# Performance work log

Measured on AMD Instinct MI355X. Metric: run time of the kernel, lower is better.

Reference implementation:

```python
import jax, jax.numpy as jnp
import numpy as np

H = 256          # h_dim
SEQ_LEN = 10     # max history length
B = 2048         # number of queries with non-empty history
N = 327680       # total flattened neighbors across all (query, timestep) segments
NUM_SEG = B * SEQ_LEN
NUM_ENT = 20000
NUM_REL = 200


def setup_inputs() -> dict:
    key = jax.random.key(0)
    ks = jax.random.split(key, 9)
    s = jax.random.randint(ks[0], (B,), 0, NUM_ENT)
    r = jax.random.randint(ks[1], (B,), 0, NUM_REL)
    nbr_ids = jax.random.randint(ks[2], (N,), 0, NUM_ENT)
    seg_ids = jnp.sort(jax.random.randint(ks[3], (N,), 0, NUM_SEG))
    ent_embeds = jax.random.normal(ks[4], (NUM_ENT, H), dtype=jnp.float32)
    rel_embeds = jax.random.normal(ks[5], (NUM_REL, H), dtype=jnp.float32)
    W_attn = jax.random.normal(ks[6], (3 * H, H), dtype=jnp.float32) * 0.05
    b_attn = jax.random.normal(ks[7], (H,), dtype=jnp.float32) * 0.05
    v_s = jax.random.normal(ks[8], (H, 1), dtype=jnp.float32) * 0.05
    return {"s": s, "r": r, "nbr_ids": nbr_ids, "seg_ids": seg_ids,
            "ent_embeds": ent_embeds, "rel_embeds": rel_embeds,
            "W_attn": W_attn, "b_attn": b_attn, "v_s": v_s}


def reference(s, r, nbr_ids, seg_ids, ent_embeds, rel_embeds, W_attn, b_attn, v_s):
    # Per-neighbor gathers. Each neighbor belongs to segment seg = q*SEQ_LEN + t.
    q = seg_ids // SEQ_LEN                              # query index per neighbor [N]
    em = ent_embeds[nbr_ids]                            # [N, H] neighbor embeddings
    s_emb = ent_embeds[s]                               # [B, H]
    r_emb = rel_embeds[r]                               # [B, H]
    ss = s_emb[q]                                       # [N, H]
    rr = r_emb[q]                                       # [N, H]
    # Score: tanh(Linear(3H -> H)) @ v_s  -> scalar per neighbor
    x = jnp.concatenate([em, ss, rr], axis=1)           # [N, 3H]
    scores = (jnp.tanh(x @ W_attn + b_attn) @ v_s)[:, 0]  # [N]
    # Segment softmax over neighbors within each (query, timestep) segment.
    m = jax.ops.segment_max(scores, seg_ids, num_segments=NUM_SEG)  # [S]
    e = jnp.exp(scores - m[seg_ids])                    # [N]
    denom = jax.ops.segment_sum(e, seg_ids, num_segments=NUM_SEG)   # [S]
    w = e / denom[seg_ids]                              # [N]
    # Weighted sum of neighbor embeddings per segment (scatter-reduce).
    agg = jax.ops.segment_sum(w[:, None] * em, seg_ids, num_segments=NUM_SEG)  # [S, H]
    counts = jax.ops.segment_sum(jnp.ones_like(scores), seg_ids, num_segments=NUM_SEG)
    mask = (counts > 0).astype(em.dtype).reshape(B, SEQ_LEN, 1)     # present timesteps
    agg = agg.reshape(B, SEQ_LEN, H)
    ss_t = jnp.broadcast_to(s_emb[:, None, :], (B, SEQ_LEN, H))
    rr_t = jnp.broadcast_to(r_emb[:, None, :], (B, SEQ_LEN, H))
    # Padded [B, SEQ_LEN, 3H] sequence tensor (rows for empty segments are zero,
    # matching the torch code's zero-initialized padded tensor). Dropout p=0.0.
    out = jnp.concatenate([agg, ss_t, rr_t], axis=2) * mask
    return out
```

## Files before the change

### kernel.cpp

```cpp
#include <hip/hip_runtime.h>
#include <hip/hip_bf16.h>

#define H 256
#define SEQ 10
#define C2LOG2E 2.8853900817779268f
#define LOG2E 1.4426950408889634f

typedef __attribute__((ext_vector_type(8))) short bf16x8;
typedef __attribute__((ext_vector_type(4))) float f32x4;

__device__ __forceinline__ unsigned short f2bf(float x) {
    union { float f; unsigned u; } v; v.f = x;
    unsigned r = v.u + 0x7fff + ((v.u >> 16) & 1);
    return (unsigned short)(r >> 16);
}
__device__ __forceinline__ float bf2f(unsigned short b) {
    union { unsigned u; float f; } v; v.u = ((unsigned)b) << 16;
    return v.f;
}
__device__ __forceinline__ float fexp2(float x) {
    return __builtin_amdgcn_exp2f(x);
}

__global__ void prep_kernel(const float* __restrict__ W,
                            unsigned short* __restrict__ Wt,
                            const int* __restrict__ seg_ids,
                            int* __restrict__ seg_start,
                            int nWt, int n, int num_seg) {
    if ((int)blockIdx.x < nWt) {
        int idx = blockIdx.x * 256 + threadIdx.x;
        if (idx >= H * 3 * H) return;
        int nn = idx / (3 * H), k = idx % (3 * H);
        Wt[idx] = f2bf(C2LOG2E * W[k * H + nn]);
    } else {
        int j = (blockIdx.x - nWt) * 256 + threadIdx.x;
        if (j >= n) return;
        int cur = seg_ids[j];
        int prev = (j == 0) ? -1 : seg_ids[j - 1];
        for (int s2 = prev + 1; s2 <= cur; s2++) seg_start[s2] = j;
        if (j == n - 1)
            for (int s2 = cur + 1; s2 <= num_seg; s2++) seg_start[s2] = n;
    }
}

__global__ void gemm_bf16_kernel(const float* __restrict__ entf,
                                 const int* __restrict__ sidx,
                                 const int* __restrict__ ridx,
                                 const float* __restrict__ rel,
                                 const unsigned short* __restrict__ Wt,
                                 const float* __restrict__ bias,
                                 unsigned short* __restrict__ comb,
                                 unsigned short* __restrict__ qpart,
                                 int nEntBlk, int M0, int M1) {
    __shared__ unsigned short As[64][40];
    bool isEnt = (int)blockIdx.x < nEntBlk;
    int m0 = (isEnt ? blockIdx.x : (blockIdx.x - nEntBlk)) * 64;
    int M = isEnt ? M0 : M1;
    int K = isEnt ? H : 2 * H;
    int k0 = isEnt ? 0 : H;
    int ldo = isEnt ? 512 : H;
    unsigned short* outp = isEnt ? comb : qpart;

    int t = threadIdx.x;
    int sr = t >> 2;
    int sc = (t & 3) * 8;
    int wave = t >> 6, lane = t & 63;
    int lr = lane & 15, lg = lane >> 4;

    f32x4 acc[4][4];
#pragma unroll
    for (int i = 0; i < 4; i++)
#pragma unroll
        for (int jn = 0; jn < 4; jn++) acc[i][jn] = (f32x4){0.f, 0.f, 0.f, 0.f};

    const unsigned short* bp[4];
#pragma unroll
    for (int bn = 0; bn < 4; bn++)
        bp[bn] = Wt + (size_t)(wave * 64 + bn * 16 + lr) * (3 * H) + k0 + lg * 8;

    for (int kk = 0; kk < K; kk += 32) {
        bf16x8 av = {};
        int gm = m0 + sr;
        if (gm < M) {
            const float* src;
            if (isEnt) {
                src = entf + (size_t)gm * H + kk + sc;
            } else {
                int k = kk + sc;
                src = (k < H) ? (entf + (size_t)sidx[gm] * H + k)
                              : (rel + (size_t)ridx[gm] * H + (k - H));
            }
            float4 f0 = *reinterpret_cast<const float4*>(src);
            float4 f1 = *reinterpret_cast<const float4*>(src + 4);
            av[0] = (short)f2bf(f0.x); av[1] = (short)f2bf(f0.y);
            av[2] = (short)f2bf(f0.z); av[3] = (short)f2bf(f0.w);
            av[4] = (short)f2bf(f1.x); av[5] = (short)f2bf(f1.y);
            av[6] = (short)f2bf(f1.z); av[7] = (short)f2bf(f1.w);
            if (isEnt)
                *reinterpret_cast<bf16x8*>(comb + (size_t)gm * 512 + 256 + kk + sc) = av;
        }
        *reinterpret_cast<bf16x8*>(&As[sr][sc]) = av;

        bf16x8 bfr[4];
#pragma unroll
        for (int bn = 0; bn < 4; bn++)
            bfr[bn] = *reinterpret_cast<const bf16x8*>(bp[bn] + kk);

        __syncthreads();
        bf16x8 afr[4];
#pragma unroll
        for (int am = 0; am < 4; am++)
            afr[am] = *reinterpret_cast<const bf16x8*>(&As[am * 16 + lr][lg * 8]);
#pragma unroll
        for (int am = 0; am < 4; am++)
#pragma unroll
            for (int bn = 0; bn < 4; bn++)
                acc[am][bn] = __builtin_amdgcn_mfma_f32_16x16x32_bf16(
                    afr[am], bfr[bn], acc[am][bn], 0, 0, 0);
        __syncthreads();
    }

#pragma unroll
    for (int bn = 0; bn < 4; bn++) {
        int col = wave * 64 + bn * 16 + lr;
        float bv = isEnt ? 0.f : C2LOG2E * bias[col];
#pragma unroll
        for (int am = 0; am < 4; am++) {
#pragma unroll
            for (int rr = 0; rr < 4; rr++) {
                int row = m0 + am * 16 + lg * 4 + rr;
                if (row < M)
                    outp[(size_t)row * ldo + col] = f2bf(acc[am][bn][rr] + bv);
            }
        }
    }
}

__global__ void __launch_bounds__(256, 4)
fused_agg_kernel(const int* __restrict__ nbr_ids,
                 const int* __restrict__ seg_start,
                 const unsigned short* __restrict__ comb,
                 const unsigned short* __restrict__ qpartbf,
                 const float* __restrict__ v_s,
                 const float* __restrict__ ent_embeds,
                 const float* __restrict__ rel_embeds,
                 const int* __restrict__ s,
                 const int* __restrict__ r,
                 float* __restrict__ out, int num_seg) {
    int wid = blockIdx.x * 4 + (threadIdx.x >> 6);
    int nw = gridDim.x * 4;
    int lane = threadIdx.x & 63;
    int g = lane >> 4, li = lane & 15;
    int cb = li * 16;
    int c4 = lane * 4;

    float vm2[16];
    float vsum = 0.f;
    {
        const float4* vp = reinterpret_cast<const float4*>(v_s + cb);
#pragma unroll
        for (int k = 0; k < 4; k++) {
            float4 tv = vp[k];
            vm2[4 * k + 0] = -2.f * tv.x; vm2[4 * k + 1] = -2.f * tv.y;
            vm2[4 * k + 2] = -2.f * tv.z; vm2[4 * k + 3] = -2.f * tv.w;
            vsum += tv.x + tv.y + tv.z + tv.w;
        }
    }

    for (int seg = wid; seg < num_seg; seg += nw) {
        int start = seg_start[seg], end = seg_start[seg + 1];
        int b = seg / SEQ;
        float* orow = out + (size_t)seg * (3 * H);

        if (start == end) {
            float4 z = {0.f, 0.f, 0.f, 0.f};
            *reinterpret_cast<float4*>(orow + c4) = z;
            *reinterpret_cast<float4*>(orow + H + c4) = z;
            *reinterpret_cast<float4*>(orow + 2 * H + c4) = z;
            continue;
        }

        float qv[16];
        {
            bf16x8 qa = *reinterpret_cast<const bf16x8*>(qpartbf + (size_t)b * H + cb);
            bf16x8 qb = *reinterpret_cast<const bf16x8*>(qpartbf + (size_t)b * H + cb + 8);
#pragma unroll
            for (int k = 0; k < 8; k++) {
                qv[k] = bf2f((unsigned short)qa[k]);
                qv[8 + k] = bf2f((unsigned short)qb[k]);
            }
        }

        float acc[16];
#pragma unroll
        for (int k = 0; k < 16; k++) acc[k] = 0.f;
        float lpart = 0.f;

        int cc = end - start;
        int nitm = (cc + 3) >> 2;

        int j0 = min(g, cc - 1);
        const unsigned short* row = comb + (size_t)nbr_ids[start + j0] * 512 + cb;
        bf16x8 p0 = *reinterpret_cast<const bf16x8*>(row);
        bf16x8 p1 = *reinterpret_cast<const bf16x8*>(row + 8);
        bf16x8 e0 = *reinterpret_cast<const bf16x8*>(row + 256);
        bf16x8 e1 = *reinterpret_cast<const bf16x8*>(row + 264);

        for (int ji = 0; ji < nitm; ji++) {
            int jn = min(4 * (ji + 1) + g, cc - 1);
            const unsigned short* rown = comb + (size_t)nbr_ids[start + jn] * 512 + cb;
            bf16x8 p0n = *reinterpret_cast<const bf16x8*>(rown);
            bf16x8 p1n = *reinterpret_cast<const bf16x8*>(rown + 8);
            bf16x8 e0n = *reinterpret_cast<const bf16x8*>(rown + 256);
            bf16x8 e1n = *reinterpret_cast<const bf16x8*>(rown + 264);

            float sa = 0.f, sb = 0.f;
#pragma unroll
            for (int k = 0; k < 8; k++) {
                sa = fmaf(vm2[k], __builtin_amdgcn_rcpf(
                        fexp2(bf2f((unsigned short)p0[k]) + qv[k]) + 1.f), sa);
                sb = fmaf(vm2[8 + k], __builtin_amdgcn_rcpf(
                        fexp2(bf2f((unsigned short)p1[k]) + qv[8 + k]) + 1.f), sb);
            }
            float s16 = sa + sb + vsum;
            s16 += __shfl_xor(s16, 1);
            s16 += __shfl_xor(s16, 2);
            s16 += __shfl_xor(s16, 4);
            s16 += __shfl_xor(s16, 8);
            float e = fexp2(s16 * LOG2E);
            e = (4 * ji + g < cc) ? e : 0.f;
            lpart += e;
#pragma unroll
            for (int k = 0; k < 8; k++) {
                acc[k] = fmaf(e, bf2f((unsigned short)e0[k]), acc[k]);
                acc[8 + k] = fmaf(e, bf2f((unsigned short)e1[k]), acc[8 + k]);
            }
            p0 = p0n; p1 = p1n; e0 = e0n; e1 = e1n;
        }

        lpart += __shfl_xor(lpart, 16);
        lpart += __shfl_xor(lpart, 32);
#pragma unroll
        for (int k = 0; k < 16; k++) {
            acc[k] += __shfl_xor(acc[k], 16);
            acc[k] += __shfl_xor(acc[k], 32);
        }
        float invl = 1.f / lpart;

        float4 o;
#pragma unroll
        for (int k = 0; k < 4; k++) {
            float v0 = acc[k], v1 = acc[4 + k], v2 = acc[8 + k], v3 = acc[12 + k];
            float pick = (g == 0) ? v0 : (g == 1) ? v1 : (g == 2) ? v2 : v3;
            if (k == 0) o.x = pick * invl;
            else if (k == 1) o.y = pick * invl;
            else if (k == 2) o.z = pick * invl;
            else o.w = pick * invl;
        }
        *reinterpret_cast<float4*>(orow + cb + 4 * g) = o;
        *reinterpret_cast<float4*>(orow + H + c4) =
            *reinterpret_cast<const float4*>(ent_embeds + (size_t)s[b] * H + c4);
        *reinterpret_cast<float4*>(orow + 2 * H + c4) =
            *reinterpret_cast<const float4*>(rel_embeds + (size_t)r[b] * H + c4);
    }
}

extern "C" void kernel_launch(void* const* d_in, const int* in_sizes, int n_in,
                              void* d_out, int out_size, void* d_ws, size_t ws_size,
                              hipStream_t stream) {
    const int* s = (const int*)d_in[0];
    const int* r = (const int*)d_in[1];
    const int* nbr_ids = (const int*)d_in[2];
    const int* seg_ids = (const int*)d_in[3];
    const float* ent_embeds = (const float*)d_in[4];
    const float* rel_embeds = (const float*)d_in[5];
    const float* W_attn = (const float*)d_in[6];
    const float* b_attn = (const float*)d_in[7];
    const float* v_s = (const float*)d_in[8];
    float* out = (float*)d_out;

    int B = in_sizes[0];
    int N = in_sizes[2];
    int num_ent = in_sizes[4] / H;
    int num_seg = B * SEQ;

    char* ws = (char*)d_ws;
    unsigned short* comb = (unsigned short*)ws;
    unsigned short* Wt = comb + (size_t)num_ent * 512;
    unsigned short* qpartbf = Wt + (size_t)H * 3 * H;
    int* seg_start = (int*)(qpartbf + (size_t)B * H);

    int nWt = (H * 3 * H + 255) / 256;
    int nSeg = (N + 255) / 256;
    prep_kernel<<<nWt + nSeg, 256, 0, stream>>>(W_attn, Wt, seg_ids, seg_start,
                                                nWt, N, num_seg);

    int nEntBlk = (num_ent + 63) / 64;
    int nQBlk = B / 64;
    gemm_bf16_kernel<<<nEntBlk + nQBlk, 256, 0, stream>>>(
        ent_embeds, s, r, rel_embeds, Wt, b_attn, comb, qpartbf,
        nEntBlk, num_ent, B);

    fused_agg_kernel<<<2048, 256, 0, stream>>>(
        nbr_ids, seg_start, comb, qpartbf, v_s,
        ent_embeds, rel_embeds, s, r, out, num_seg);
}
```

Measured before the change: 93.70 us.

## Assign one wave per segment, pair sigmoid reciprocals, predicate tail gathers

Replaces the persistent grid-stride loop in the aggregation kernel with one wave per segment: 128-thread blocks, a grid sized to the segment count, and looser launch bounds. The query-side ent/rel rows are now loaded early so their latency overlaps the neighbor loop. Out-of-range neighbor gathers are skipped by predication instead of clamped to the last row. The tanh score math now combines two sigmoid terms over one reciprocal, halving rcp instructions at the cost of extra multiplies and some risk to precision. Launch overhead grows with many more small blocks, and the register bound changes.

```diff
diff --git a/kernel.cpp b/kernel.cpp
--- a/kernel.cpp
+++ b/kernel.cpp
@@ -136,7 +136,7 @@
     }
 }
 
-__global__ void __launch_bounds__(256, 4)
+__global__ void __launch_bounds__(128)
 fused_agg_kernel(const int* __restrict__ nbr_ids,
                  const int* __restrict__ seg_start,
                  const unsigned short* __restrict__ comb,
@@ -147,12 +147,26 @@
                  const int* __restrict__ s,
                  const int* __restrict__ r,
                  float* __restrict__ out, int num_seg) {
-    int wid = blockIdx.x * 4 + (threadIdx.x >> 6);
-    int nw = gridDim.x * 4;
+    int seg = blockIdx.x * 2 + (threadIdx.x >> 6);
+    if (seg >= num_seg) return;
     int lane = threadIdx.x & 63;
     int g = lane >> 4, li = lane & 15;
     int cb = li * 16;
     int c4 = lane * 4;
+    int b = seg / SEQ;
+    int start = seg_start[seg], end = seg_start[seg + 1];
+    float* orow = out + (size_t)seg * (3 * H);
+
+    if (start == end) {
+        float4 z = {0.f, 0.f, 0.f, 0.f};
+        *reinterpret_cast<float4*>(orow + c4) = z;
+        *reinterpret_cast<float4*>(orow + H + c4) = z;
+        *reinterpret_cast<float4*>(orow + 2 * H + c4) = z;
+        return;
+    }
+
+    float4 ssv = *reinterpret_cast<const float4*>(ent_embeds + (size_t)s[b] * H + c4);
+    float4 rrv = *reinterpret_cast<const float4*>(rel_embeds + (size_t)r[b] * H + c4);
 
     float vm2[16];
     float vsum = 0.f;
@@ -167,102 +181,97 @@
         }
     }
 
-    for (int seg = wid; seg < num_seg; seg += nw) {
-        int start = seg_start[seg], end = seg_start[seg + 1];
-        int b = seg / SEQ;
-        float* orow = out + (size_t)seg * (3 * H);
-
-        if (start == end) {
-            float4 z = {0.f, 0.f, 0.f, 0.f};
-            *reinterpret_cast<float4*>(orow + c4) = z;
-            *reinterpret_cast<float4*>(orow + H + c4) = z;
-            *reinterpret_cast<float4*>(orow + 2 * H + c4) = z;
-            continue;
-        }
-
-        float qv[16];
-        {
-            bf16x8 qa = *reinterpret_cast<const bf16x8*>(qpartbf + (size_t)b * H + cb);
-            bf16x8 qb = *reinterpret_cast<const bf16x8*>(qpartbf + (size_t)b * H + cb + 8);
-#pragma unroll
-            for (int k = 0; k < 8; k++) {
-                qv[k] = bf2f((unsigned short)qa[k]);
-                qv[8 + k] = bf2f((unsigned short)qb[k]);
-            }
-        }
-
-        float acc[16];
-#pragma unroll
-        for (int k = 0; k < 16; k++) acc[k] = 0.f;
-        float lpart = 0.f;
-
-        int cc = end - start;
-        int nitm = (cc + 3) >> 2;
-
-        int j0 = min(g, cc - 1);
-        const unsigned short* row = comb + (size_t)nbr_ids[start + j0] * 512 + cb;
-        bf16x8 p0 = *reinterpret_cast<const bf16x8*>(row);
-        bf16x8 p1 = *reinterpret_cast<const bf16x8*>(row + 8);
-        bf16x8 e0 = *reinterpret_cast<const bf16x8*>(row + 256);
-        bf16x8 e1 = *reinterpret_cast<const bf16x8*>(row + 264);
-
-        for (int ji = 0; ji < nitm; ji++) {
-            int jn = min(4 * (ji + 1) + g, cc - 1);
+    float qv[16];
+    {
+        bf16x8 qa = *reinterpret_cast<const bf16x8*>(qpartbf + (size_t)b * H + cb);
+        bf16x8 qb = *reinterpret_cast<const bf16x8*>(qpartbf + (size_t)b * H + cb + 8);
+#pragma unroll
+        for (int k = 0; k < 8; k++) {
+            qv[k] = bf2f((unsigned short)qa[k]);
+            qv[8 + k] = bf2f((unsigned short)qb[k]);
+        }
+    }
+
+    float acc[16];
+#pragma unroll
+    for (int k = 0; k < 16; k++) acc[k] = 0.f;
+    float lpart = 0.f;
+
+    int cc = end - start;
+    int nitm = (cc + 3) >> 2;
+
+    bf16x8 p0 = {}, p1 = {}, e0 = {}, e1 = {};
+    if (g < cc) {
+        const unsigned short* row = comb + (size_t)nbr_ids[start + g] * 512 + cb;
+        p0 = *reinterpret_cast<const bf16x8*>(row);
+        p1 = *reinterpret_cast<const bf16x8*>(row + 8);
+        e0 = *reinterpret_cast<const bf16x8*>(row + 256);
+        e1 = *reinterpret_cast<const bf16x8*>(row + 264);
+    }
+
+    for (int ji = 0; ji < nitm; ji++) {
+        bf16x8 p0n = {}, p1n = {}, e0n = {}, e1n = {};
+        int jn = 4 * (ji + 1) + g;
+        if (jn < cc) {
             const unsigned short* rown = comb + (size_t)nbr_ids[start + jn] * 512 + cb;
-            bf16x8 p0n = *reinterpret_cast<const bf16x8*>(rown);
-            bf16x8 p1n = *reinterpret_cast<const bf16x8*>(rown + 8);
-            bf16x8 e0n = *reinterpret_cast<const bf16x8*>(rown + 256);
-            bf16x8 e1n = *reinterpret_cast<const bf16x8*>(rown + 264);
-
-            float sa = 0.f, sb = 0.f;
-#pragma unroll
-            for (int k = 0; k < 8; k++) {
-                sa = fmaf(vm2[k], __builtin_amdgcn_rcpf(
-                        fexp2(bf2f((unsigned short)p0[k]) + qv[k]) + 1.f), sa);
-                sb = fmaf(vm2[8 + k], __builtin_amdgcn_rcpf(
-                        fexp2(bf2f((unsigned short)p1[k]) + qv[8 + k]) + 1.f), sb);
-            }
-            float s16 = sa + sb + vsum;
-            s16 += __shfl_xor(s16, 1);
-            s16 += __shfl_xor(s16, 2);
-            s16 += __shfl_xor(s16, 4);
-            s16 += __shfl_xor(s16, 8);
-            float e = fexp2(s16 * LOG2E);
-            e = (4 * ji + g < cc) ? e : 0.f;
-            lpart += e;
-#pragma unroll
-            for (int k = 0; k < 8; k++) {
-                acc[k] = fmaf(e, bf2f((unsigned short)e0[k]), acc[k]);
-                acc[8 + k] = fmaf(e, bf2f((unsigned short)e1[k]), acc[8 + k]);
-            }
-            p0 = p0n; p1 = p1n; e0 = e0n; e1 = e1n;
-        }
-
-        lpart += __shfl_xor(lpart, 16);
-        lpart += __shfl_xor(lpart, 32);
-#pragma unroll
-        for (int k = 0; k < 16; k++) {
-            acc[k] += __shfl_xor(acc[k], 16);
-            acc[k] += __shfl_xor(acc[k], 32);
-        }
-        float invl = 1.f / lpart;
-
-        float4 o;
-#pragma unroll
-        for (int k = 0; k < 4; k++) {
-            float v0 = acc[k], v1 = acc[4 + k], v2 = acc[8 + k], v3 = acc[12 + k];
-            float pick = (g == 0) ? v0 : (g == 1) ? v1 : (g == 2) ? v2 : v3;
-            if (k == 0) o.x = pick * invl;
-            else if (k == 1) o.y = pick * invl;
-            else if (k == 2) o.z = pick * invl;
-            else o.w = pick * invl;
-        }
-        *reinterpret_cast<float4*>(orow + cb + 4 * g) = o;
-        *reinterpret_cast<float4*>(orow + H + c4) =
-            *reinterpret_cast<const float4*>(ent_embeds + (size_t)s[b] * H + c4);
-        *reinterpret_cast<float4*>(orow + 2 * H + c4) =
-            *reinterpret_cast<const float4*>(rel_embeds + (size_t)r[b] * H + c4);
-    }
+            p0n = *reinterpret_cast<const bf16x8*>(rown);
+            p1n = *reinterpret_cast<const bf16x8*>(rown + 8);
+            e0n = *reinterpret_cast<const bf16x8*>(rown + 256);
+            e1n = *reinterpret_cast<const bf16x8*>(rown + 264);
+        }
+
+        float sa = 0.f, sb = 0.f;
+#pragma unroll
+        for (int k = 0; k < 8; k += 2) {
+            float a0 = fexp2(bf2f((unsigned short)p0[k]) + qv[k]) + 1.f;
+            float a1 = fexp2(bf2f((unsigned short)p1[k]) + qv[8 + k]) + 1.f;
+            float num = vm2[k] * a1;
+            num = fmaf(vm2[8 + k], a0, num);
+            sa = fmaf(num, __builtin_amdgcn_rcpf(a0 * a1), sa);
+            float b0 = fexp2(bf2f((unsigned short)p0[k + 1]) + qv[k + 1]) + 1.f;
+            float b1 = fexp2(bf2f((unsigned short)p1[k + 1]) + qv[9 + k]) + 1.f;
+            float numb = vm2[k + 1] * b1;
+            numb = fmaf(vm2[9 + k], b0, numb);
+            sb = fmaf(numb, __builtin_amdgcn_rcpf(b0 * b1), sb);
+        }
+        float s16 = sa + sb + vsum;
+        s16 += __shfl_xor(s16, 1);
+        s16 += __shfl_xor(s16, 2);
+        s16 += __shfl_xor(s16, 4);
+        s16 += __shfl_xor(s16, 8);
+        float e = fexp2(s16 * LOG2E);
+        e = (4 * ji + g < cc) ? e : 0.f;
+        lpart += e;
+#pragma unroll
+        for (int k = 0; k < 8; k++) {
+            acc[k] = fmaf(e, bf2f((unsigned short)e0[k]), acc[k]);
+            acc[8 + k] = fmaf(e, bf2f((unsigned short)e1[k]), acc[8 + k]);
+        }
+        p0 = p0n; p1 = p1n; e0 = e0n; e1 = e1n;
+    }
+
+    lpart += __shfl_xor(lpart, 16);
+    lpart += __shfl_xor(lpart, 32);
+#pragma unroll
+    for (int k = 0; k < 16; k++) {
+        acc[k] += __shfl_xor(acc[k], 16);
+        acc[k] += __shfl_xor(acc[k], 32);
+    }
+    float invl = 1.f / lpart;
+
+    float4 o;
+#pragma unroll
+    for (int k = 0; k < 4; k++) {
+        float v0 = acc[k], v1 = acc[4 + k], v2 = acc[8 + k], v3 = acc[12 + k];
+        float pick = (g == 0) ? v0 : (g == 1) ? v1 : (g == 2) ? v2 : v3;
+        if (k == 0) o.x = pick * invl;
+        else if (k == 1) o.y = pick * invl;
+        else if (k == 2) o.z = pick * invl;
+        else o.w = pick * invl;
+    }
+    *reinterpret_cast<float4*>(orow + cb + 4 * g) = o;
+    *reinterpret_cast<float4*>(orow + H + c4) = ssv;
+    *reinterpret_cast<float4*>(orow + 2 * H + c4) = rrv;
 }
 
 extern "C" void kernel_launch(void* const* d_in, const int* in_sizes, int n_in,
@@ -301,7 +310,7 @@
         ent_embeds, s, r, rel_embeds, Wt, b_attn, comb, qpartbf,
         nEntBlk, num_ent, B);
 
-    fused_agg_kernel<<<2048, 256, 0, stream>>>(
+    fused_agg_kernel<<<(num_seg + 1) / 2, 128, 0, stream>>>(
         nbr_ids, seg_start, comb, qpartbf, v_s,
         ent_embeds, rel_embeds, s, r, out, num_seg);
 }
```

After: 91.22 us. 2.6% less time.
